# Optimization experiments

Hardware: AMD Instinct MI355X
Metric: run time of the kernel (lower is better)

Reference implementation:

```python
import jax, jax.numpy as jnp
import numpy as np

LGRAD = 27.8   # gradient scale (module _lgrad)
LCOL = 10.0    # color scale   (module _lcol)
MAXLVL = 4     # merge levels  (module _maxlvl)
FINAL_TH = 0.0 # merge threshold (module _final_th)


def _grad_mag(feat):
    # per-pixel gradient magnitude, averaged over channels -> [B,H,W]
    gx = jnp.pad(feat[..., :, 1:] - feat[..., :, :-1], ((0, 0), (0, 0), (0, 0), (0, 1)))
    gy = jnp.pad(feat[..., 1:, :] - feat[..., :-1, :], ((0, 0), (0, 0), (0, 1), (0, 0)))
    return jnp.sqrt(gx * gx + gy * gy + 1e-12).mean(axis=1)


def _edges(H, W):
    # directed 4-connectivity edge list over the pixel grid (static, numpy)
    idx = np.arange(H * W).reshape(H, W)
    hu, hv = idx[:, :-1].ravel(), idx[:, 1:].ravel()
    vu, vv = idx[:-1, :].ravel(), idx[1:, :].ravel()
    src = np.concatenate([hu, hv, vu, vv]).astype(np.int32)
    dst = np.concatenate([hv, hu, vv, vu]).astype(np.int32)
    return jnp.asarray(src), jnp.asarray(dst)


def _merge_level(labels, pix, gmag, src, dst, N):
    # labels [N] int32 pixel->region, pix [N,3], gmag [N]
    ones = jnp.ones_like(gmag)
    cnt = jax.ops.segment_sum(ones, labels, num_segments=N)
    csum = jax.ops.segment_sum(pix, labels, num_segments=N)
    gsum = jax.ops.segment_sum(gmag, labels, num_segments=N)
    safe = jnp.maximum(cnt, 1.0)
    mcol = csum / safe[:, None]      # region mean color [N,3]
    mg = gsum / safe                 # region mean gradient [N]

    la, lb = labels[src], labels[dst]
    valid = la != lb
    dc = jnp.sqrt(jnp.sum((mcol[la] - mcol[lb]) ** 2, axis=-1) + 1e-12)
    ge = 0.5 * (mg[la] + mg[lb])
    sim = jnp.exp(-(dc / LCOL + ge / LGRAD))     # in (0,1], higher = more similar
    sim = jnp.where(valid, sim, -1.0)

    best = jax.ops.segment_max(sim, la, num_segments=N)     # best-neighbor similarity
    cand = jnp.where(valid & (sim == best[la]), lb, jnp.int32(N))
    bn = jax.ops.segment_min(cand, la, num_segments=N)      # deterministic best neighbor id

    r = jnp.arange(N, dtype=jnp.int32)
    bnc = jnp.clip(bn, 0, N - 1)
    mutual = (bn < N) & (bnc[bnc] == r) & (best > FINAL_TH)  # mutual-best, cycle-free pairs
    parent = jnp.where(mutual, jnp.minimum(r, bnc), r)
    return parent[labels]


def _tokenize(feat):
    B, C, H, W = feat.shape
    N = H * W
    gmag = _grad_mag(feat).reshape(B, N)
    pix = feat.reshape(B, C, N).transpose(0, 2, 1)            # [B,N,3]
    src, dst = _edges(H, W)
    labels = jnp.broadcast_to(jnp.arange(N, dtype=jnp.int32), (B, N))

    step = jax.vmap(lambda l, p, g: _merge_level(l, p, g, src, dst, N))
    for _ in range(MAXLVL):
        labels = step(labels, pix, gmag)

    def mean_map(l, p):
        cnt = jax.ops.segment_sum(jnp.ones((N,), p.dtype), l, num_segments=N)
        cs = jax.ops.segment_sum(p, l, num_segments=N)
        return (cs / jnp.maximum(cnt, 1.0)[:, None])[l]

    colmap = jax.vmap(mean_map)(labels, pix)                  # [B,N,3] region-mean colors
    colmap = colmap.transpose(0, 2, 1).reshape(B, C, H, W)
    return labels.reshape(B, H, W), colmap


def setup_inputs() -> dict:
    key = jax.random.key(0)
    feat = jax.random.uniform(key, (8, 3, 512, 512), dtype=jnp.float32) * 255.0
    return {"feat": feat}


def reference(feat):
    return _tokenize(feat)
```

## Files before the change

### kernel.cpp

```cpp
#include <hip/hip_runtime.h>
#include <math.h>

#define WW 512
#define HH 512
#define NPIX (WW*HH)
#define NSH 18
#define NXCD 8

typedef unsigned long long u64;
typedef unsigned int u32;
typedef unsigned short u16;

__device__ __forceinline__ u64 umax64(u64 a, u64 b) { return a > b ? a : b; }

__device__ __forceinline__ int swz_idx() {
  int g = gridDim.x;
  int b = (int)blockIdx.x;
  int nb2 = (b & (NXCD - 1)) * (g >> 3) + (b >> 3);
  return nb2 * 256 + (int)threadIdx.x;
}

__device__ __forceinline__ void tile_coords(int& bb, int& x0, int& y0) {
  int g = gridDim.x;
  int b = (int)blockIdx.x;
  int t = (b & (NXCD - 1)) * (g >> 3) + (b >> 3);
  bb = t >> 10;
  int rem = t & 1023;
  y0 = (rem >> 4) << 3;
  x0 = (rem & 15) << 5;
}

__device__ __forceinline__ float d_colg(const float* __restrict__ fb, int p, int pw, int ph,
                                        float col[3]) {
  float s = 0.f;
#pragma unroll
  for (int c = 0; c < 3; ++c) {
    const float* fc = fb + (size_t)c * NPIX;
    float v = fc[p];
    col[c] = v;
    float gx = (pw < WW - 1) ? __fsub_rn(fc[p + 1], v) : 0.f;
    float gy = (ph < HH - 1) ? __fsub_rn(fc[p + WW], v) : 0.f;
    float g = __fsqrt_rn(__fadd_rn(__fadd_rn(__fmul_rn(gx, gx), __fmul_rn(gy, gy)), 1e-12f));
    s = __fadd_rn(s, g);
  }
  return __fdiv_rn(s, 3.0f);
}

__device__ __forceinline__ u64 d_simbits(float4 a, float4 b) {
  float d0 = __fsub_rn(a.x, b.x);
  float d1 = __fsub_rn(a.y, b.y);
  float d2 = __fsub_rn(a.z, b.z);
  float ss = __fadd_rn(__fadd_rn(__fmul_rn(d0, d0), __fmul_rn(d1, d1)), __fmul_rn(d2, d2));
  float dc = __fsqrt_rn(__fadd_rn(ss, 1e-12f));
  float ge = __fmul_rn(0.5f, __fadd_rn(a.w, b.w));
  float t = __fadd_rn(__fdiv_rn(dc, 10.0f), __fdiv_rn(ge, 27.8f));
  float sim = (float)exp(-(double)t);
  return ((u64)__float_as_uint(sim)) << 32;
}

__global__ __launch_bounds__(256) void k_prep0edge(const float* __restrict__ feat,
                                                   int* __restrict__ labels,
                                                   int* __restrict__ cnt,
                                                   float4* __restrict__ pix4,
                                                   float4* __restrict__ mcol4,
                                                   u64* __restrict__ bnkey) {
  __shared__ float4 scolg[340];
  __shared__ u64 skey[256];
  int bb, x0, y0;
  tile_coords(bb, x0, y0);
  const float* fb = feat + (size_t)bb * 3 * NPIX;
  int tid = (int)threadIdx.x;
  skey[tid] = 0;
  for (int c = tid; c < 340; c += 256) {
    int cx = (c % 34) - 1, cy = (c / 34) - 1;
    int x = x0 + cx, y = y0 + cy;
    if (x >= 0 && x < WW && y >= 0 && y < HH) {
      float col[3];
      float g = d_colg(fb, y * WW + x, x, y, col);
      scolg[c] = make_float4(col[0], col[1], col[2], g);
    }
  }
  __syncthreads();
  int tx = tid & 31, ty = tid >> 5;
  int x = x0 + tx, y = y0 + ty;
  int n = y * WW + x;
  int idx = (bb << NSH) + n;
  int cell = (ty + 1) * 34 + (tx + 1);
  float4 ca = scolg[cell];
  labels[idx] = n;
  cnt[idx] = 1;
  pix4[idx] = ca;
  mcol4[idx] = ca;
  u64 key = 0;
  if (x < WW - 1) {
    u64 s = d_simbits(ca, scolg[cell + 1]);
    key = umax64(key, s | (u32)(NPIX - (n + 1)));
    if (tx < 31) atomicMax(&skey[tid + 1], s | (u32)(NPIX - n));
  }
  if (tx == 0 && x > 0) {
    u64 s = d_simbits(ca, scolg[cell - 1]);
    key = umax64(key, s | (u32)(NPIX - (n - 1)));
  }
  if (y < HH - 1) {
    u64 s = d_simbits(ca, scolg[cell + 34]);
    key = umax64(key, s | (u32)(NPIX - (n + WW)));
    if (ty < 7) atomicMax(&skey[tid + 32], s | (u32)(NPIX - n));
  }
  if (ty == 0 && y > 0) {
    u64 s = d_simbits(ca, scolg[cell - 34]);
    key = umax64(key, s | (u32)(NPIX - (n - WW)));
  }
  __syncthreads();
  bnkey[idx] = umax64(key, skey[tid]);
}

__global__ __launch_bounds__(256) void k_edge(const int* __restrict__ labels,
                                              const float4* __restrict__ mcol4,
                                              u64* __restrict__ bnext) {
  __shared__ int sla[256];
  __shared__ float4 sma[256];
  __shared__ u64 skey[256];
  int bb, x0, y0;
  tile_coords(bb, x0, y0);
  int tid = (int)threadIdx.x;
  int tx = tid & 31, ty = tid >> 5;
  int x = x0 + tx, y = y0 + ty;
  int n = y * WW + x;
  int base = bb << NSH;
  int idx = base + n;
  int la = labels[idx];
  float4 ma = mcol4[base + la];
  sla[tid] = la;
  sma[tid] = ma;
  skey[tid] = 0;
  __syncthreads();
  u64 key = 0;
  if (x < WW - 1) {
    if (tx < 31) {
      int lb = sla[tid + 1];
      if (lb != la) {
        u64 s = d_simbits(ma, sma[tid + 1]);
        key = umax64(key, s | (u32)(NPIX - lb));
        atomicMax(&skey[tid + 1], s | (u32)(NPIX - la));
      }
    } else {
      int lb = labels[idx + 1];
      if (lb != la) key = umax64(key, d_simbits(ma, mcol4[base + lb]) | (u32)(NPIX - lb));
    }
  }
  if (tx == 0 && x > 0) {
    int lb = labels[idx - 1];
    if (lb != la) key = umax64(key, d_simbits(ma, mcol4[base + lb]) | (u32)(NPIX - lb));
  }
  if (y < HH - 1) {
    if (ty < 7) {
      int lb = sla[tid + 32];
      if (lb != la) {
        u64 s = d_simbits(ma, sma[tid + 32]);
        key = umax64(key, s | (u32)(NPIX - lb));
        atomicMax(&skey[tid + 32], s | (u32)(NPIX - la));
      }
    } else {
      int lb = labels[idx + WW];
      if (lb != la) key = umax64(key, d_simbits(ma, mcol4[base + lb]) | (u32)(NPIX - lb));
    }
  }
  if (ty == 0 && y > 0) {
    int lb = labels[idx - WW];
    if (lb != la) key = umax64(key, d_simbits(ma, mcol4[base + lb]) | (u32)(NPIX - lb));
  }
  __syncthreads();
  u64 val = umax64(key, skey[tid]);
  if (val) atomicMax(&bnext[base + la], val);
}

template<bool LVL0, bool ZNEXT>
__global__ __launch_bounds__(256) void k_scanpairs(int* __restrict__ labels,
                                                   int* __restrict__ cnt,
                                                   u16* __restrict__ mem,
                                                   const u64* __restrict__ bnkey,
                                                   u64* __restrict__ bnext,
                                                   const float4* __restrict__ pix4,
                                                   float4* __restrict__ mcol4, int total) {
  __shared__ u64 swl[256];
  __shared__ int scnt;
  if (threadIdx.x == 0) scnt = 0;
  __syncthreads();

  int idx = swz_idx();
  if (ZNEXT && idx < total) bnext[idx] = 0;
  bool pred = false;
  u64 e = 0;
  if (idx < total) {
    int n = idx & (NPIX - 1);
    int base = idx - n;
    int c = 1;
    bool live = true;
    if (!LVL0) { c = cnt[idx]; live = (c > 0); }
    if (live) {
      u64 K = bnkey[idx];
      int v = NPIX - (int)(K & 0xffffffffu);
      if (v < NPIX && n < v) {
        u64 Kv = bnkey[base + v];
        if (NPIX - (int)(Kv & 0xffffffffu) == n) {
          pred = true;
          e = ((u64)(u32)idx << 32) | ((u64)(u32)c << 18) | (u32)v;
        }
      }
    }
  }

  u64 mask = __ballot(pred);
  int lane = (int)(threadIdx.x & 63);
  int wb0 = 0;
  if (lane == 0 && mask) wb0 = atomicAdd(&scnt, __popcll(mask));
  int wb = __shfl(wb0, 0);
  if (pred) {
    int pos = wb + __popcll(mask & ((1ull << lane) - 1ull));
    swl[pos] = e;
  }
  __syncthreads();
  int m = scnt;
  if ((int)threadIdx.x >= m) return;

  e = swl[threadIdx.x];
  int idx2 = (int)(e >> 32);
  int v = (int)(e & 0x3ffffu);
  int n = idx2 & (NPIX - 1);
  int base = idx2 - n;
  float s0, s1, s2, sg;
  int k;
  u16* mo = mem + ((size_t)idx2 << 4);
  if (LVL0) {
    k = 2;
    float4 pa = pix4[idx2];
    float4 pb = pix4[base + v];
    s0 = __fadd_rn(__fadd_rn(0.f, pa.x), pb.x);
    s1 = __fadd_rn(__fadd_rn(0.f, pa.y), pb.y);
    s2 = __fadd_rn(__fadd_rn(0.f, pa.z), pb.z);
    sg = __fadd_rn(__fadd_rn(0.f, pa.w), pb.w);
    mo[0] = 0; mo[1] = (u16)(v - n);
    labels[idx2] = n;
    labels[base + v] = n;
  } else {
    int c = (int)((e >> 18) & 0x1fu);
    int cb = cnt[base + v];
    const u16* ma = mem + ((size_t)idx2 << 4);
    const u16* mb = mem + ((size_t)(base + v) << 4);
    k = c + cb;
    s0 = s1 = s2 = sg = 0.f;
    int i = 0, j = 0;
    while (i < c || j < cb) {
      int av = (i < c) ? ((c == 1) ? n : n + (int)ma[i]) : 0x7fffffff;
      int bv = (j < cb) ? ((cb == 1) ? v : v + (int)mb[j]) : 0x7fffffff;
      int x;
      if (av < bv) { x = av; ++i; } else { x = bv; ++j; }
      float4 p = pix4[base + x];
      s0 = __fadd_rn(s0, p.x);
      s1 = __fadd_rn(s1, p.y);
      s2 = __fadd_rn(s2, p.z);
      sg = __fadd_rn(sg, p.w);
      labels[base + x] = n;
    }
    int i2 = c - 1, j2 = cb - 1;
    for (int t2 = k - 1; t2 >= 0; --t2) {
      int av = (i2 >= 0) ? ((c == 1) ? n : n + (int)ma[i2]) : (int)0x80000000;
      int bv = (j2 >= 0) ? ((cb == 1) ? v : v + (int)mb[j2]) : (int)0x80000000;
      int x;
      if (av > bv) { x = av; --i2; } else { x = bv; --j2; }
      mo[t2] = (u16)(x - n);
    }
  }
  float safe = (float)k;
  mcol4[idx2] = make_float4(__fdiv_rn(s0, safe), __fdiv_rn(s1, safe),
                            __fdiv_rn(s2, safe), __fdiv_rn(sg, safe));
  cnt[idx2] = k;
  cnt[base + v] = 0;
}

__global__ __launch_bounds__(256) void k_out(const int* __restrict__ labels,
                                             const float4* __restrict__ mcol4,
                                             float* __restrict__ out, int total,
                                             int b0, int Btot) {
  int idx = swz_idx();
  if (idx >= total) return;
  int b = idx >> NSH;
  int n = idx & (NPIX - 1);
  int l = labels[idx];
  out[(size_t)(b0 + b) * NPIX + n] = (float)l;
  size_t cb = (size_t)Btot * NPIX;
  float4 m = mcol4[(size_t)(b << NSH) + l];
  out[cb + ((size_t)(b0 + b) * 3 + 0) * NPIX + n] = m.x;
  out[cb + ((size_t)(b0 + b) * 3 + 1) * NPIX + n] = m.y;
  out[cb + ((size_t)(b0 + b) * 3 + 2) * NPIX + n] = m.z;
}

extern "C" void kernel_launch(void* const* d_in, const int* in_sizes, int n_in,
                              void* d_out, int out_size, void* d_ws, size_t ws_size,
                              hipStream_t stream) {
  const float* feat = (const float*)d_in[0];
  float* out = (float*)d_out;
  int Btot = in_sizes[0] / (3 * NPIX);

  const size_t perB = (size_t)NPIX * 88;
  int nbmax = (int)(ws_size / perB);
  if (nbmax < 1) nbmax = 1;
  if (nbmax > Btot) nbmax = Btot;

  for (int b0 = 0; b0 < Btot; b0 += nbmax) {
    int nb = (Btot - b0 < nbmax) ? (Btot - b0) : nbmax;
    size_t cn = (size_t)nb << NSH;
    char* p = (char*)d_ws;
    float4* mcol4 = (float4*)p; p += cn * 16;
    float4* pix4 = (float4*)p;  p += cn * 16;
    u64* keyA = (u64*)p;        p += cn * 8;
    u64* keyB = (u64*)p;        p += cn * 8;
    int* labels = (int*)p;      p += cn * 4;
    int* cnt = (int*)p;         p += cn * 4;
    u16* mem = (u16*)p;

    const float* fchunk = feat + (size_t)b0 * 3 * NPIX;
    int total = (int)cn;
    int grid = total >> 8;

    k_prep0edge<<<grid, 256, 0, stream>>>(fchunk, labels, cnt, pix4, mcol4, keyA);
    k_scanpairs<true, true><<<grid, 256, 0, stream>>>(labels, cnt, mem, keyA, keyB,
                                                      pix4, mcol4, total);
    k_edge<<<grid, 256, 0, stream>>>(labels, mcol4, keyB);
    k_scanpairs<false, true><<<grid, 256, 0, stream>>>(labels, cnt, mem, keyB, keyA,
                                                       pix4, mcol4, total);
    k_edge<<<grid, 256, 0, stream>>>(labels, mcol4, keyA);
    k_scanpairs<false, true><<<grid, 256, 0, stream>>>(labels, cnt, mem, keyA, keyB,
                                                       pix4, mcol4, total);
    k_edge<<<grid, 256, 0, stream>>>(labels, mcol4, keyB);
    k_scanpairs<false, false><<<grid, 256, 0, stream>>>(labels, cnt, mem, keyB, keyA,
                                                        pix4, mcol4, total);
    k_out<<<grid, 256, 0, stream>>>(labels, mcol4, out, total, b0, Btot);
  }
}
```

Measured before the change: 305.9 us.

## Tag best-neighbor keys with level bits to drop key zeroing and buffer

```diff
diff --git a/kernel.cpp b/kernel.cpp
--- a/kernel.cpp
+++ b/kernel.cpp
@@ -116,7 +116,7 @@
 
 __global__ __launch_bounds__(256) void k_edge(const int* __restrict__ labels,
                                               const float4* __restrict__ mcol4,
-                                              u64* __restrict__ bnext) {
+                                              u64* __restrict__ bnkey, int lvl) {
   __shared__ int sla[256];
   __shared__ float4 sma[256];
   __shared__ u64 skey[256];
@@ -171,40 +171,38 @@
   }
   __syncthreads();
   u64 val = umax64(key, skey[tid]);
-  if (val) atomicMax(&bnext[base + la], val);
-}
-
-template<bool LVL0, bool ZNEXT>
+  if (val) atomicMax(&bnkey[base + la], ((u64)lvl << 62) | val);
+}
+
+template<bool LVL0, bool LAST>
 __global__ __launch_bounds__(256) void k_scanpairs(int* __restrict__ labels,
                                                    int* __restrict__ cnt,
                                                    u16* __restrict__ mem,
                                                    const u64* __restrict__ bnkey,
-                                                   u64* __restrict__ bnext,
                                                    const float4* __restrict__ pix4,
-                                                   float4* __restrict__ mcol4, int total) {
+                                                   float4* __restrict__ mcol4,
+                                                   int total, int lvl) {
   __shared__ u64 swl[256];
   __shared__ int scnt;
   if (threadIdx.x == 0) scnt = 0;
   __syncthreads();
 
   int idx = swz_idx();
-  if (ZNEXT && idx < total) bnext[idx] = 0;
   bool pred = false;
   u64 e = 0;
   if (idx < total) {
     int n = idx & (NPIX - 1);
     int base = idx - n;
-    int c = 1;
-    bool live = true;
-    if (!LVL0) { c = cnt[idx]; live = (c > 0); }
-    if (live) {
-      u64 K = bnkey[idx];
+    u64 K = bnkey[idx];
+    bool valid = LVL0 ? true : ((int)(K >> 62) == lvl);
+    if (valid) {
       int v = NPIX - (int)(K & 0xffffffffu);
       if (v < NPIX && n < v) {
         u64 Kv = bnkey[base + v];
-        if (NPIX - (int)(Kv & 0xffffffffu) == n) {
+        bool pv = LVL0 ? true : ((int)(Kv >> 62) == lvl);
+        if (pv && NPIX - (int)(Kv & 0xffffffffu) == n) {
           pred = true;
-          e = ((u64)(u32)idx << 32) | ((u64)(u32)c << 18) | (u32)v;
+          e = ((u64)(u32)idx << 32) | (u32)v;
         }
       }
     }
@@ -225,7 +223,7 @@
 
   e = swl[threadIdx.x];
   int idx2 = (int)(e >> 32);
-  int v = (int)(e & 0x3ffffu);
+  int v = (int)(e & 0xffffffffu);
   int n = idx2 & (NPIX - 1);
   int base = idx2 - n;
   float s0, s1, s2, sg;
@@ -243,7 +241,7 @@
     labels[idx2] = n;
     labels[base + v] = n;
   } else {
-    int c = (int)((e >> 18) & 0x1fu);
+    int c = cnt[idx2];
     int cb = cnt[base + v];
     const u16* ma = mem + ((size_t)idx2 << 4);
     const u16* mb = mem + ((size_t)(base + v) << 4);
@@ -260,25 +258,32 @@
       s1 = __fadd_rn(s1, p.y);
       s2 = __fadd_rn(s2, p.z);
       sg = __fadd_rn(sg, p.w);
-      labels[base + x] = n;
-    }
-    int i2 = c - 1, j2 = cb - 1;
-    for (int t2 = k - 1; t2 >= 0; --t2) {
-      int av = (i2 >= 0) ? ((c == 1) ? n : n + (int)ma[i2]) : (int)0x80000000;
-      int bv = (j2 >= 0) ? ((cb == 1) ? v : v + (int)mb[j2]) : (int)0x80000000;
-      int x;
-      if (av > bv) { x = av; --i2; } else { x = bv; --j2; }
-      mo[t2] = (u16)(x - n);
+      if (!LAST) labels[base + x] = n;
+    }
+    if (!LAST) {
+      int i2 = c - 1, j2 = cb - 1;
+      for (int t2 = k - 1; t2 >= 0; --t2) {
+        int av = (i2 >= 0) ? ((c == 1) ? n : n + (int)ma[i2]) : (int)0x80000000;
+        int bv = (j2 >= 0) ? ((cb == 1) ? v : v + (int)mb[j2]) : (int)0x80000000;
+        int x;
+        if (av > bv) { x = av; --i2; } else { x = bv; --j2; }
+        mo[t2] = (u16)(x - n);
+      }
     }
   }
   float safe = (float)k;
   mcol4[idx2] = make_float4(__fdiv_rn(s0, safe), __fdiv_rn(s1, safe),
                             __fdiv_rn(s2, safe), __fdiv_rn(sg, safe));
-  cnt[idx2] = k;
-  cnt[base + v] = 0;
+  if (LAST) {
+    cnt[base + v] = -n;
+  } else {
+    cnt[idx2] = k;
+    cnt[base + v] = 0;
+  }
 }
 
 __global__ __launch_bounds__(256) void k_out(const int* __restrict__ labels,
+                                             const int* __restrict__ cnt,
                                              const float4* __restrict__ mcol4,
                                              float* __restrict__ out, int total,
                                              int b0, int Btot) {
@@ -286,10 +291,13 @@
   if (idx >= total) return;
   int b = idx >> NSH;
   int n = idx & (NPIX - 1);
+  int base = b << NSH;
   int l = labels[idx];
+  int c2 = cnt[base + l];
+  if (c2 <= 0) l = -c2;
   out[(size_t)(b0 + b) * NPIX + n] = (float)l;
   size_t cb = (size_t)Btot * NPIX;
-  float4 m = mcol4[(size_t)(b << NSH) + l];
+  float4 m = mcol4[base + l];
   out[cb + ((size_t)(b0 + b) * 3 + 0) * NPIX + n] = m.x;
   out[cb + ((size_t)(b0 + b) * 3 + 1) * NPIX + n] = m.y;
   out[cb + ((size_t)(b0 + b) * 3 + 2) * NPIX + n] = m.z;
@@ -302,7 +310,7 @@
   float* out = (float*)d_out;
   int Btot = in_sizes[0] / (3 * NPIX);
 
-  const size_t perB = (size_t)NPIX * 88;
+  const size_t perB = (size_t)NPIX * 80;
   int nbmax = (int)(ws_size / perB);
   if (nbmax < 1) nbmax = 1;
   if (nbmax > Btot) nbmax = Btot;
@@ -313,8 +321,7 @@
     char* p = (char*)d_ws;
     float4* mcol4 = (float4*)p; p += cn * 16;
     float4* pix4 = (float4*)p;  p += cn * 16;
-    u64* keyA = (u64*)p;        p += cn * 8;
-    u64* keyB = (u64*)p;        p += cn * 8;
+    u64* key = (u64*)p;         p += cn * 8;
     int* labels = (int*)p;      p += cn * 4;
     int* cnt = (int*)p;         p += cn * 4;
     u16* mem = (u16*)p;
@@ -323,18 +330,18 @@
     int total = (int)cn;
     int grid = total >> 8;
 
-    k_prep0edge<<<grid, 256, 0, stream>>>(fchunk, labels, cnt, pix4, mcol4, keyA);
-    k_scanpairs<true, true><<<grid, 256, 0, stream>>>(labels, cnt, mem, keyA, keyB,
-                                                      pix4, mcol4, total);
-    k_edge<<<grid, 256, 0, stream>>>(labels, mcol4, keyB);
-    k_scanpairs<false, true><<<grid, 256, 0, stream>>>(labels, cnt, mem, keyB, keyA,
-                                                       pix4, mcol4, total);
-    k_edge<<<grid, 256, 0, stream>>>(labels, mcol4, keyA);
-    k_scanpairs<false, true><<<grid, 256, 0, stream>>>(labels, cnt, mem, keyA, keyB,
-                                                       pix4, mcol4, total);
-    k_edge<<<grid, 256, 0, stream>>>(labels, mcol4, keyB);
-    k_scanpairs<false, false><<<grid, 256, 0, stream>>>(labels, cnt, mem, keyB, keyA,
-                                                        pix4, mcol4, total);
-    k_out<<<grid, 256, 0, stream>>>(labels, mcol4, out, total, b0, Btot);
-  }
-}
+    k_prep0edge<<<grid, 256, 0, stream>>>(fchunk, labels, cnt, pix4, mcol4, key);
+    k_scanpairs<true, false><<<grid, 256, 0, stream>>>(labels, cnt, mem, key,
+                                                       pix4, mcol4, total, 0);
+    k_edge<<<grid, 256, 0, stream>>>(labels, mcol4, key, 1);
+    k_scanpairs<false, false><<<grid, 256, 0, stream>>>(labels, cnt, mem, key,
+                                                        pix4, mcol4, total, 1);
+    k_edge<<<grid, 256, 0, stream>>>(labels, mcol4, key, 2);
+    k_scanpairs<false, false><<<grid, 256, 0, stream>>>(labels, cnt, mem, key,
+                                                        pix4, mcol4, total, 2);
+    k_edge<<<grid, 256, 0, stream>>>(labels, mcol4, key, 3);
+    k_scanpairs<false, true><<<grid, 256, 0, stream>>>(labels, cnt, mem, key,
+                                                       pix4, mcol4, total, 3);
+    k_out<<<grid, 256, 0, stream>>>(labels, cnt, mcol4, out, total, b0, Btot);
+  }
+}
```

After: 292.2 us. 4.5% less time.
